# Kernel tuning notes

Measured on AMD Instinct MI355X. Metric: run time of the kernel, lower is better.

## Reference

```python
import jax, jax.numpy as jnp
import numpy as np

N_NODES = 10000
N_EDGES = 640000
D_FEAT = 128


def setup_inputs() -> dict:
    key = jax.random.key(0)
    k1, k2, k3, k4 = jax.random.split(key, 4)
    feat = jax.random.normal(k1, (N_NODES, D_FEAT), dtype=jnp.float32)
    src = jax.random.randint(k2, (N_EDGES,), 0, N_NODES, dtype=jnp.int32)
    dst = jax.random.randint(k3, (N_EDGES,), 0, N_NODES, dtype=jnp.int32)
    W = jax.random.normal(k4, (D_FEAT, D_FEAT), dtype=jnp.float32) / np.sqrt(D_FEAT).astype(np.float32)
    b = jnp.zeros((D_FEAT,), dtype=jnp.float32)
    return {"feat": feat, "W": W, "b": b, "src": src, "dst": dst}


def reference(feat, W, b, src, dst):
    eps = jnp.float32(0.0)  # init_eps=0, learn_eps=False (buffer)
    n = feat.shape[0]
    # message passing: copy_u('h','m') + sum reducer -> neigh[i] = sum_{j->i} h_j
    h_src = feat[src]                                   # [E, D] gather
    neigh = jax.ops.segment_sum(h_src, dst, num_segments=n)  # [N, D] scatter-add
    rst = (1.0 + eps) * feat + neigh
    # apply_func: Linear(D, D)
    rst = rst @ W + b
    # per-edge score: e = sum(h_src * tanh(h_dst), axis=1)
    e = jnp.sum(h_src * jnp.tanh(feat[dst]), axis=1)    # [E]
    # edge_softmax: softmax over edges grouped by destination node
    m = jax.ops.segment_max(e, dst, num_segments=n)     # [N]
    e_exp = jnp.exp(e - m[dst])
    denom = jax.ops.segment_sum(e_exp, dst, num_segments=n)  # [N]
    e_soft = e_exp / denom[dst]
    return rst, e_soft
```

## Files before the change

kernel.cpp:

```cpp
#include <hip/hip_runtime.h>
#include <hip/hip_bf16.h>
#include <math.h>

#define N_NODES 10000
#define N_EDGES 640000
#define D_FEAT  128
#define SLOT    128
#define MAXDEG  128


__device__ __forceinline__ unsigned bf16rne2(float a, float b) {
    unsigned ua = __float_as_uint(a);
    unsigned ub = __float_as_uint(b);
    unsigned ra = (ua + 0x7fffu + ((ua >> 16) & 1u)) >> 16;
    unsigned rb = (ub + 0x7fffu + ((ub >> 16) & 1u)) >> 16;
    return ra | (rb << 16);
}

__global__ void scatter_build(const int* __restrict__ dst,
                              const float* __restrict__ feat,
                              int* __restrict__ cnt,
                              unsigned* __restrict__ slot_u,
                              unsigned short* __restrict__ feat_bf) {
    int tid = blockIdx.x * 256 + threadIdx.x;

    {
        int t8 = tid * 8;
        float4 f0 = *(const float4*)&feat[t8];
        float4 f1 = *(const float4*)&feat[t8 + 4];
        uint4 p;
        p.x = bf16rne2(f0.x, f0.y);
        p.y = bf16rne2(f0.z, f0.w);
        p.z = bf16rne2(f1.x, f1.y);
        p.w = bf16rne2(f1.z, f1.w);
        *(uint4*)&feat_bf[t8] = p;
    }

    int i0 = tid * 4;
    int4 d4 = *(const int4*)&dst[i0];
    int p0 = atomicAdd(&cnt[d4.x << 4], 1);
    int p1 = atomicAdd(&cnt[d4.y << 4], 1);
    int p2 = atomicAdd(&cnt[d4.z << 4], 1);
    int p3 = atomicAdd(&cnt[d4.w << 4], 1);
    slot_u[d4.x * SLOT + p0] = (unsigned)(i0 + 0);
    slot_u[d4.y * SLOT + p1] = (unsigned)(i0 + 1);
    slot_u[d4.z * SLOT + p2] = (unsigned)(i0 + 2);
    slot_u[d4.w * SLOT + p3] = (unsigned)(i0 + 3);
}

__device__ __forceinline__ float cvt_acc_dot(uint4 U, float4 t0, float4 t1,
                                             float4& a0, float4& a1) {
    float v0 = __uint_as_float(U.x << 16);
    float v1 = __uint_as_float(U.x & 0xffff0000u);
    float v2 = __uint_as_float(U.y << 16);
    float v3 = __uint_as_float(U.y & 0xffff0000u);
    float v4 = __uint_as_float(U.z << 16);
    float v5 = __uint_as_float(U.z & 0xffff0000u);
    float v6 = __uint_as_float(U.w << 16);
    float v7 = __uint_as_float(U.w & 0xffff0000u);
    a0.x += v0; a0.y += v1; a0.z += v2; a0.w += v3;
    a1.x += v4; a1.y += v5; a1.z += v6; a1.w += v7;
    return v0 * t0.x + v1 * t0.y + v2 * t0.z + v3 * t0.w
         + v4 * t1.x + v5 * t1.y + v6 * t1.z + v7 * t1.w;
}

__global__ void fused_node(const float* __restrict__ feat,
                           const unsigned short* __restrict__ feat_bf,
                           const int* __restrict__ src,
                           const int* __restrict__ cnt,
                           const unsigned* __restrict__ slot_u,
                           float* __restrict__ out_e,
                           float* __restrict__ x_out) {
    __shared__ float t_sh[4][D_FEAT];
    __shared__ float e_sh[4][MAXDEG];
    int wv = threadIdx.x >> 6;
    int lane = threadIdx.x & 63;
    int node = blockIdx.x * 4 + wv;
    if (node >= N_NODES) return;

    int g = lane >> 4;
    int l = lane & 15;

    int deg = cnt[node << 4];
    int dm = (deg > 0) ? deg - 1 : 0;
    unsigned base = (unsigned)node * SLOT;

    float2 fd2 = ((const float2*)(feat + (size_t)node * D_FEAT))[lane];
    ((float2*)&t_sh[wv][0])[lane] = make_float2(tanhf(fd2.x), tanhf(fd2.y));
    float4 t0 = ((const float4*)&t_sh[wv][0])[l * 2];
    float4 t1 = ((const float4*)&t_sh[wv][0])[l * 2 + 1];

    unsigned e0id = slot_u[base + min(lane, dm)];
    unsigned e1id = slot_u[base + min(64 + lane, dm)];
    int m0 = src[min(e0id, (unsigned)(N_EDGES - 1))];
    int m1 = src[min(e1id, (unsigned)(N_EDGES - 1))];

    float4 acc0 = make_float4(0.f, 0.f, 0.f, 0.f);
    float4 acc1 = make_float4(0.f, 0.f, 0.f, 0.f);

    int nsteps = (deg + 7) >> 3;

    #define LOAD_STEP(T, U0, U1)                                              \
        {                                                                     \
            int m_ = ((T) < 8) ? m0 : m1;                                     \
            int s0_ = __shfl(m_, ((T) * 8 + g) & 63, 64);                     \
            int s1_ = __shfl(m_, ((T) * 8 + 4 + g) & 63, 64);                 \
            U0 = *((const uint4*)(feat_bf + (size_t)s0_ * D_FEAT) + l);       \
            U1 = *((const uint4*)(feat_bf + (size_t)s1_ * D_FEAT) + l);       \
        }

    #define PROC_STEP(T, U0, U1)                                              \
        {                                                                     \
            int i0_ = (T) * 8 + g;                                            \
            int i1_ = i0_ + 4;                                                \
            if ((((T) + 1) << 3) <= deg) {                                    \
                float d0 = cvt_acc_dot(U0, t0, t1, acc0, acc1);               \
                float d1 = cvt_acc_dot(U1, t0, t1, acc0, acc1);               \
                _Pragma("unroll")                                             \
                for (int off = 1; off <= 8; off <<= 1) {                      \
                    d0 += __shfl_xor(d0, off, 64);                            \
                    d1 += __shfl_xor(d1, off, 64);                            \
                }                                                             \
                if (l == 0) {                                                 \
                    e_sh[wv][i0_] = d0;                                       \
                    e_sh[wv][i1_] = d1;                                       \
                }                                                             \
            } else {                                                          \
                bool a0_ = i0_ < deg, a1_ = i1_ < deg;                        \
                if (!a0_) U0 = make_uint4(0u, 0u, 0u, 0u);                    \
                if (!a1_) U1 = make_uint4(0u, 0u, 0u, 0u);                    \
                float d0 = cvt_acc_dot(U0, t0, t1, acc0, acc1);               \
                float d1 = cvt_acc_dot(U1, t0, t1, acc0, acc1);               \
                _Pragma("unroll")                                             \
                for (int off = 1; off <= 8; off <<= 1) {                      \
                    d0 += __shfl_xor(d0, off, 64);                            \
                    d1 += __shfl_xor(d1, off, 64);                            \
                }                                                             \
                if (a0_ && l == 0) e_sh[wv][i0_] = d0;                        \
                if (a1_ && l == 0) e_sh[wv][i1_] = d1;                        \
            }                                                                 \
        }

    uint4 A0, A1, B0, B1, C0, C1, D0, D1;
    if (nsteps > 0) LOAD_STEP(0, A0, A1);
    if (nsteps > 1) LOAD_STEP(1, B0, B1);
    if (nsteps > 2) LOAD_STEP(2, C0, C1);
    if (nsteps > 3) LOAD_STEP(3, D0, D1);

    for (int t = 0; t < nsteps; t += 4) {
        PROC_STEP(t, A0, A1);
        if (t + 4 < nsteps) LOAD_STEP(t + 4, A0, A1);
        if (t + 1 < nsteps) {
            PROC_STEP(t + 1, B0, B1);
            if (t + 5 < nsteps) LOAD_STEP(t + 5, B0, B1);
        }
        if (t + 2 < nsteps) {
            PROC_STEP(t + 2, C0, C1);
            if (t + 6 < nsteps) LOAD_STEP(t + 6, C0, C1);
        }
        if (t + 3 < nsteps) {
            PROC_STEP(t + 3, D0, D1);
            if (t + 7 < nsteps) LOAD_STEP(t + 7, D0, D1);
        }
    }
    #undef LOAD_STEP
    #undef PROC_STEP

    #pragma unroll
    for (int off = 16; off <= 32; off <<= 1) {
        acc0.x += __shfl_xor(acc0.x, off, 64);
        acc0.y += __shfl_xor(acc0.y, off, 64);
        acc0.z += __shfl_xor(acc0.z, off, 64);
        acc0.w += __shfl_xor(acc0.w, off, 64);
        acc1.x += __shfl_xor(acc1.x, off, 64);
        acc1.y += __shfl_xor(acc1.y, off, 64);
        acc1.z += __shfl_xor(acc1.z, off, 64);
        acc1.w += __shfl_xor(acc1.w, off, 64);
    }

    float2 mp = (g == 0) ? make_float2(acc0.x, acc0.y)
              : (g == 1) ? make_float2(acc0.z, acc0.w)
              : (g == 2) ? make_float2(acc1.x, acc1.y)
              :            make_float2(acc1.z, acc1.w);
    int p2 = l * 4 + g;
    float2 fn = ((const float2*)(feat + (size_t)node * D_FEAT))[p2];
    ((float2*)(x_out + (size_t)node * D_FEAT))[p2] =
        make_float2(mp.x + fn.x, mp.y + fn.y);

    float mx = -INFINITY;
    for (int i = lane; i < deg; i += 64) mx = fmaxf(mx, e_sh[wv][i]);
    #pragma unroll
    for (int off = 32; off; off >>= 1)
        mx = fmaxf(mx, __shfl_xor(mx, off, 64));

    float sum = 0.f;
    for (int i = lane; i < deg; i += 64) {
        float ex = expf(e_sh[wv][i] - mx);
        e_sh[wv][i] = ex;
        sum += ex;
    }
    #pragma unroll
    for (int off = 32; off; off >>= 1)
        sum += __shfl_xor(sum, off, 64);

    float inv = 1.0f / sum;
    if (lane < deg)      out_e[e0id] = e_sh[wv][lane] * inv;
    if (64 + lane < deg) out_e[e1id] = e_sh[wv][64 + lane] * inv;
}

__global__ void node_gemm(float* __restrict__ io,
                          const float* __restrict__ W,
                          const float* __restrict__ b) {
    __shared__ float xst[D_FEAT][20];
    int rbase = blockIdx.x * 16;

    for (int i = threadIdx.x; i < 16 * D_FEAT; i += 256) {
        int r = i >> 7, c = i & 127;
        xst[c][r] = io[(size_t)(rbase + r) * D_FEAT + c];
    }
    __syncthreads();

    int tc = threadIdx.x & 63;
    int rh = threadIdx.x >> 6;
    float a00 = 0.f, a01 = 0.f, a10 = 0.f, a11 = 0.f;
    float a20 = 0.f, a21 = 0.f, a30 = 0.f, a31 = 0.f;

    for (int k = 0; k < D_FEAT; ++k) {
        float2 xa = *(const float2*)&xst[k][rh * 4];
        float2 xb = *(const float2*)&xst[k][rh * 4 + 2];
        float2 w  = *(const float2*)&W[(size_t)k * D_FEAT + tc * 2];
        a00 += xa.x * w.x; a01 += xa.x * w.y;
        a10 += xa.y * w.x; a11 += xa.y * w.y;
        a20 += xb.x * w.x; a21 += xb.x * w.y;
        a30 += xb.y * w.x; a31 += xb.y * w.y;
    }
    __syncthreads();

    float2 bias = *(const float2*)&b[tc * 2];
    int rw = rbase + rh * 4;
    ((float2*)&io[(size_t)(rw + 0) * D_FEAT])[tc] = make_float2(a00 + bias.x, a01 + bias.y);
    ((float2*)&io[(size_t)(rw + 1) * D_FEAT])[tc] = make_float2(a10 + bias.x, a11 + bias.y);
    ((float2*)&io[(size_t)(rw + 2) * D_FEAT])[tc] = make_float2(a20 + bias.x, a21 + bias.y);
    ((float2*)&io[(size_t)(rw + 3) * D_FEAT])[tc] = make_float2(a30 + bias.x, a31 + bias.y);
}

extern "C" void kernel_launch(void* const* d_in, const int* in_sizes, int n_in,
                              void* d_out, int out_size, void* d_ws, size_t ws_size,
                              hipStream_t stream) {
    const float* feat = (const float*)d_in[0];
    const float* W    = (const float*)d_in[1];
    const float* b    = (const float*)d_in[2];
    const int*   src  = (const int*)d_in[3];
    const int*   dst  = (const int*)d_in[4];

    float* out_rst = (float*)d_out;
    float* out_e   = (float*)d_out + (size_t)N_NODES * D_FEAT;

    char* ws = (char*)d_ws;
    int*            cnt     = (int*)(ws + 0);
    unsigned*       slot_u  = (unsigned*)(ws + 640000);
    unsigned short* feat_bf = (unsigned short*)(ws + 5760000);

    hipMemsetAsync(cnt, 0, 640000, stream);

    scatter_build<<<N_EDGES / 4 / 256, 256, 0, stream>>>(dst, feat, cnt, slot_u, feat_bf);

    fused_node<<<(N_NODES + 3) / 4, 256, 0, stream>>>(feat, feat_bf, src, cnt,
                                                      slot_u, out_e, out_rst);

    node_gemm<<<N_NODES / 16, 256, 0, stream>>>(out_rst, W, b);
}
```

Before: 146.3 us.

## Store source ids in CSR slots and write edge scores via slot-to-edge map

The bucket build now stores each edge's 16-bit source node id directly in the per-destination slot and records each edge's slot position. This removes the dependent src[] gather in the node kernel. Softmax results are written contiguously per slot, then gathered into edge order by extra blocks appended to the GEMM kernel, which replaces the scattered per-edge writes. In exchange the build pass now processes one edge per thread, and the extra edge pass adds random reads and a larger workspace.

```diff
diff --git a/kernel.cpp b/kernel.cpp
--- a/kernel.cpp
+++ b/kernel.cpp
@@ -17,14 +17,16 @@
     return ra | (rb << 16);
 }
 
-__global__ void scatter_build(const int* __restrict__ dst,
+__global__ void scatter_build(const int* __restrict__ src,
+                              const int* __restrict__ dst,
                               const float* __restrict__ feat,
                               int* __restrict__ cnt,
-                              unsigned* __restrict__ slot_u,
+                              unsigned short* __restrict__ slot_us,
+                              int* __restrict__ pos_by_edge,
                               unsigned short* __restrict__ feat_bf) {
     int tid = blockIdx.x * 256 + threadIdx.x;
 
-    {
+    if (tid < (N_NODES * D_FEAT) / 8) {
         int t8 = tid * 8;
         float4 f0 = *(const float4*)&feat[t8];
         float4 f1 = *(const float4*)&feat[t8 + 4];
@@ -36,16 +38,12 @@
         *(uint4*)&feat_bf[t8] = p;
     }
 
-    int i0 = tid * 4;
-    int4 d4 = *(const int4*)&dst[i0];
-    int p0 = atomicAdd(&cnt[d4.x << 4], 1);
-    int p1 = atomicAdd(&cnt[d4.y << 4], 1);
-    int p2 = atomicAdd(&cnt[d4.z << 4], 1);
-    int p3 = atomicAdd(&cnt[d4.w << 4], 1);
-    slot_u[d4.x * SLOT + p0] = (unsigned)(i0 + 0);
-    slot_u[d4.y * SLOT + p1] = (unsigned)(i0 + 1);
-    slot_u[d4.z * SLOT + p2] = (unsigned)(i0 + 2);
-    slot_u[d4.w * SLOT + p3] = (unsigned)(i0 + 3);
+    int d = dst[tid];
+    int s = src[tid];
+    int pos = atomicAdd(&cnt[d << 4], 1);
+    int idx = d * SLOT + pos;
+    slot_us[idx] = (unsigned short)s;
+    pos_by_edge[tid] = idx;
 }
 
 __device__ __forceinline__ float cvt_acc_dot(uint4 U, float4 t0, float4 t1,
@@ -66,10 +64,9 @@
 
 __global__ void fused_node(const float* __restrict__ feat,
                            const unsigned short* __restrict__ feat_bf,
-                           const int* __restrict__ src,
                            const int* __restrict__ cnt,
-                           const unsigned* __restrict__ slot_u,
-                           float* __restrict__ out_e,
+                           const unsigned short* __restrict__ slot_us,
+                           float* __restrict__ e_slot,
                            float* __restrict__ x_out) {
     __shared__ float t_sh[4][D_FEAT];
     __shared__ float e_sh[4][MAXDEG];
@@ -90,10 +87,8 @@
     float4 t0 = ((const float4*)&t_sh[wv][0])[l * 2];
     float4 t1 = ((const float4*)&t_sh[wv][0])[l * 2 + 1];
 
-    unsigned e0id = slot_u[base + min(lane, dm)];
-    unsigned e1id = slot_u[base + min(64 + lane, dm)];
-    int m0 = src[min(e0id, (unsigned)(N_EDGES - 1))];
-    int m1 = src[min(e1id, (unsigned)(N_EDGES - 1))];
+    int m0 = (int)slot_us[base + min(lane, dm)];
+    int m1 = (int)slot_us[base + min(64 + lane, dm)];
 
     float4 acc0 = make_float4(0.f, 0.f, 0.f, 0.f);
     float4 acc1 = make_float4(0.f, 0.f, 0.f, 0.f);
@@ -204,13 +199,28 @@
         sum += __shfl_xor(sum, off, 64);
 
     float inv = 1.0f / sum;
-    if (lane < deg)      out_e[e0id] = e_sh[wv][lane] * inv;
-    if (64 + lane < deg) out_e[e1id] = e_sh[wv][64 + lane] * inv;
-}
-
-__global__ void node_gemm(float* __restrict__ io,
-                          const float* __restrict__ W,
-                          const float* __restrict__ b) {
+    for (int i = lane; i < deg; i += 64)
+        e_slot[base + i] = e_sh[wv][i] * inv;
+}
+
+__global__ void gemm_and_edge(float* __restrict__ io,
+                              const float* __restrict__ W,
+                              const float* __restrict__ b,
+                              const int* __restrict__ pos_by_edge,
+                              const float* __restrict__ e_slot,
+                              float* __restrict__ out_e) {
+    if (blockIdx.x >= 625) {
+        int i4 = ((blockIdx.x - 625) * 256 + threadIdx.x) * 4;
+        int4 p = *(const int4*)&pos_by_edge[i4];
+        float4 r;
+        r.x = e_slot[p.x];
+        r.y = e_slot[p.y];
+        r.z = e_slot[p.z];
+        r.w = e_slot[p.w];
+        *(float4*)&out_e[i4] = r;
+        return;
+    }
+
     __shared__ float xst[D_FEAT][20];
     int rbase = blockIdx.x * 16;
 
@@ -257,16 +267,19 @@
     float* out_e   = (float*)d_out + (size_t)N_NODES * D_FEAT;
 
     char* ws = (char*)d_ws;
-    int*            cnt     = (int*)(ws + 0);
-    unsigned*       slot_u  = (unsigned*)(ws + 640000);
-    unsigned short* feat_bf = (unsigned short*)(ws + 5760000);
+    int*            cnt         = (int*)(ws + 0);
+    unsigned short* slot_us     = (unsigned short*)(ws + 640000);
+    float*          e_slot      = (float*)(ws + 3200000);
+    int*            pos_by_edge = (int*)(ws + 8320000);
+    unsigned short* feat_bf     = (unsigned short*)(ws + 10880000);
 
     hipMemsetAsync(cnt, 0, 640000, stream);
 
-    scatter_build<<<N_EDGES / 4 / 256, 256, 0, stream>>>(dst, feat, cnt, slot_u, feat_bf);
-
-    fused_node<<<(N_NODES + 3) / 4, 256, 0, stream>>>(feat, feat_bf, src, cnt,
-                                                      slot_u, out_e, out_rst);
-
-    node_gemm<<<N_NODES / 16, 256, 0, stream>>>(out_rst, W, b);
-}
+    scatter_build<<<N_EDGES / 256, 256, 0, stream>>>(src, dst, feat, cnt,
+                                                     slot_us, pos_by_edge, feat_bf);
+
+    fused_node<<<(N_NODES + 3) / 4, 256, 0, stream>>>(feat, feat_bf, cnt,
+                                                      slot_us, e_slot, out_rst);
+
+    gemm_and_edge<<<1250, 256, 0, stream>>>(out_rst, W, b, pos_by_edge, e_slot, out_e);
+}
```

New measurement: 139.7 us. 4.5% less time.
